# Optimization experiments

Measured on AMD Instinct MI355X. Metric: run time of the kernel, lower is better.

Reference implementation:

```python
import jax, jax.numpy as jnp
import numpy as np

B, N, C, H = 4, 2048, 768, 12
D = C // H  # head_dim = 64


def setup_inputs() -> dict:
    key = jax.random.key(0)
    ks = jax.random.split(key, 16)
    s = 1.0 / np.sqrt(C)
    inp = {
        "x1": jax.random.normal(ks[0], (B, N, C), jnp.float32),
        "x2": jax.random.normal(ks[1], (B, N, C), jnp.float32),
        "mask_1": jax.random.uniform(ks[2], (B, N), jnp.float32),
        "mask_2": jax.random.uniform(ks[3], (B, N), jnp.float32),
        "Wq": jax.random.normal(ks[4], (C, C), jnp.float32) * s,
        "bq": jnp.zeros((C,), jnp.float32),
        "Wk": jax.random.normal(ks[5], (C, C), jnp.float32) * s,
        "bk": jnp.zeros((C,), jnp.float32),
        "Wv": jax.random.normal(ks[6], (C, C), jnp.float32) * s,
        "bv": jnp.zeros((C,), jnp.float32),
        "Wo": jax.random.normal(ks[7], (C, C), jnp.float32) * s,
        "bo": jnp.zeros((C,), jnp.float32),
        "temperature": jnp.asarray(1.0, jnp.float32),
        "ln_gamma": jnp.ones((C,), jnp.float32),
        "ln_beta": jnp.zeros((C,), jnp.float32),
    }
    return inp


def _layernorm(x, gamma, beta, eps=1e-5):
    mu = jnp.mean(x, axis=-1, keepdims=True)
    var = jnp.var(x, axis=-1, keepdims=True)
    return (x - mu) * jax.lax.rsqrt(var + eps) * gamma + beta


def reference(x1, x2, mask_1, mask_2, Wq, bq, Wk, bk, Wv, bv, Wo, bo,
              temperature, ln_gamma, ln_beta):
    # projections (nn.Linear: x @ W^T + b)
    q = (x1 @ Wq.T + bq).reshape(B, N, H, D).transpose(0, 2, 1, 3)  # [B,H,N,D]
    k = (x2 @ Wk.T + bk).reshape(B, N, H, D).transpose(0, 2, 1, 3)
    v = (x2 @ Wv.T + bv).reshape(B, N, H, D).transpose(0, 2, 1, 3)

    scores = jnp.einsum("bhnd,bhmd->bhnm", q, k) / jnp.sqrt(jnp.float32(D))
    # relative confidence bias: (mask_1[b,n] - mask_2[b,m]) / temperature
    rel = (mask_1[:, :, None] - mask_2[:, None, :]) / temperature  # [B,N,N]
    scores = scores + rel[:, None, :, :]

    attn = jax.nn.softmax(scores, axis=-1)  # dropout = identity (eval mode)
    out = jnp.einsum("bhnm,bhmd->bhnd", attn, v)
    out = out.transpose(0, 2, 1, 3).reshape(B, N, C)
    out = out @ Wo.T + bo
    return _layernorm(0.5 * x1 + out, ln_gamma, ln_beta)
```

## Files before the change

kernel.cpp:

```cpp
#include <hip/hip_runtime.h>
#include <stdint.h>

#define B_ 4
#define N_ 2048
#define C_ 768
#define H_ 12
#define D_ 64
#define NTOK 8192

typedef short bf16x8 __attribute__((ext_vector_type(8)));
typedef float f32x4 __attribute__((ext_vector_type(4)));
typedef float f32x16 __attribute__((ext_vector_type(16)));
typedef unsigned short ushort8 __attribute__((ext_vector_type(8)));
typedef unsigned short u16x4 __attribute__((ext_vector_type(4)));

__device__ __forceinline__ unsigned short f2bf(float f) {
  union { float f; unsigned u; } v; v.f = f;
  unsigned r = v.u + 0x7FFFu + ((v.u >> 16) & 1u);
  return (unsigned short)(r >> 16);
}

__device__ __forceinline__ void load_lds16(const void* g, void* lds_base) {
  __builtin_amdgcn_global_load_lds(
      (const __attribute__((address_space(1))) unsigned int*)g,
      (__attribute__((address_space(3))) unsigned int*)(uint32_t)(uintptr_t)lds_base,
      16, 0, 0);
}

__device__ __forceinline__ int key2slot(int key) {
  return ((key >> 5) << 5) | (((key >> 4) & 1) << 4) | (((key >> 2) & 1) << 3)
       | (((key >> 3) & 1) << 2) | (key & 3);
}

__device__ __forceinline__ bf16x8 pack8(const float* p) {
  union { unsigned u[4]; bf16x8 v; } r;
#pragma unroll
  for (int j=0;j<4;j++) {
    union { float f; unsigned u; } a, b;
    a.f = p[2*j]; b.f = p[2*j+1];
    r.u[j] = __builtin_amdgcn_perm(b.u + 0x8000u, a.u + 0x8000u, 0x07060302u);
  }
  return r.v;
}

__global__ __launch_bounds__(256) void cvt6(
    const float* s0, const float* s1, const float* s2, const float* s3,
    const float* s4, const float* s5,
    unsigned short* d0, unsigned short* d1, unsigned short* d2,
    unsigned short* d3, unsigned short* d4, unsigned short* d5,
    int n01, int n25)
{
  int y = blockIdx.y;
  const float* s = (y==0)?s0:(y==1)?s1:(y==2)?s2:(y==3)?s3:(y==4)?s4:s5;
  unsigned short* d = (y==0)?d0:(y==1)?d1:(y==2)?d2:(y==3)?d3:(y==4)?d4:d5;
  int n = (y<2) ? n01 : n25;
  int i = (blockIdx.x*256 + threadIdx.x)*8;
  if (i >= n) return;
  float4 f0 = *(const float4*)(s+i);
  float4 f1 = *(const float4*)(s+i+4);
  ushort8 o;
  o[0]=f2bf(f0.x); o[1]=f2bf(f0.y); o[2]=f2bf(f0.z); o[3]=f2bf(f0.w);
  o[4]=f2bf(f1.x); o[5]=f2bf(f1.y); o[6]=f2bf(f1.z); o[7]=f2bf(f1.w);
  *(ushort8*)(d+i) = o;
}

__device__ __forceinline__ void gemm_core(const unsigned short* A, const unsigned short* W,
                                          int rowBase, int colBase, f32x4 (&acc)[4][4],
                                          unsigned short* As, unsigned short* Bs)
{
  int tid = threadIdx.x, wave = tid>>6, lane = tid&63, quad = lane>>4, l16 = lane&15;
  int wm = wave>>1, wn = wave&1;
  for (int k0 = 0; k0 < 768; k0 += 32) {
    __syncthreads();
#pragma unroll
    for (int p = 0; p < 2; ++p) {
      int c = p*256 + wave*64 + lane;
      load_lds16(A + (size_t)(rowBase + (c>>2))*768 + k0 + (c&3)*8,
                 As + (size_t)(p*256 + wave*64)*8);
      load_lds16(W + (size_t)(colBase + (c>>2))*768 + k0 + (c&3)*8,
                 Bs + (size_t)(p*256 + wave*64)*8);
    }
    __syncthreads();
    bf16x8 af[4], bw[4];
#pragma unroll
    for (int i=0;i<4;i++) af[i] = *(const bf16x8*)(As + (wm*64 + i*16 + l16)*32 + quad*8);
#pragma unroll
    for (int j=0;j<4;j++) bw[j] = *(const bf16x8*)(Bs + (wn*64 + j*16 + l16)*32 + quad*8);
#pragma unroll
    for (int i=0;i<4;i++)
#pragma unroll
      for (int j=0;j<4;j++)
        acc[i][j] = __builtin_amdgcn_mfma_f32_16x16x32_bf16(af[i], bw[j], acc[i][j], 0,0,0);
  }
}

__global__ __launch_bounds__(256) void qkv_gemm(
    const unsigned short* xb1, const unsigned short* xb2,
    const unsigned short* Wq, const unsigned short* Wk, const unsigned short* Wv,
    const float* bq, const float* bk, const float* bv,
    unsigned short* Qb, unsigned short* Kb, unsigned short* Vb)
{
  __shared__ unsigned short SU[64*132];
  unsigned short* As = SU;
  unsigned short* Bs = SU + 4096;
  int z = blockIdx.z;
  const unsigned short* A = (z==0) ? xb1 : xb2;
  const unsigned short* W = (z==0) ? Wq : (z==1) ? Wk : Wv;
  const float* bias       = (z==0) ? bq : (z==1) ? bk : bv;
  unsigned short* out     = (z==0) ? Qb : (z==1) ? Kb : Vb;
  int rowBase = blockIdx.x*128, colBase = blockIdx.y*128;
  int tid = threadIdx.x, wave = tid>>6, lane = tid&63, quad = lane>>4, l16 = lane&15;
  int wm = wave>>1, wn = wave&1;
  f32x4 acc[4][4] = {};
  gemm_core(A, W, rowBase, colBase, acc, As, Bs);
  if (z == 2) {
    unsigned short* T = SU;
    int b = rowBase >> 11, n0 = rowBase & 2047;
#pragma unroll
    for (int phase=0; phase<2; ++phase) {
      __syncthreads();
      if (wn == phase) {
#pragma unroll
        for (int i=0;i<4;i++)
#pragma unroll
          for (int j=0;j<4;j++) {
            int d = j*16 + l16;
            float bv_ = bias[colBase + phase*64 + d];
#pragma unroll
            for (int r=0;r<4;r++) {
              int t = wm*64 + i*16 + quad*4 + r;
              int sl = (t & 64) | key2slot(t & 63);
              T[d*132 + sl] = f2bf(acc[i][j][r] + bv_);
            }
          }
      }
      __syncthreads();
      int h = (colBase >> 6) + phase;
      int row = tid >> 2, seg = tid & 3;
      unsigned short* dst = out + ((size_t)(b*H_ + h)*D_ + row)*N_ + n0 + seg*32;
      const unsigned short* src = T + row*132 + seg*32;
#pragma unroll
      for (int u=0;u<4;u++)
        *(ushort8*)(dst + u*8) = *(const ushort8*)(src + u*8);
    }
  } else {
#pragma unroll
    for (int i=0;i<4;i++)
#pragma unroll
      for (int j=0;j<4;j++) {
        int col = colBase + wn*64 + j*16 + l16;
        float bv_ = bias[col];
        int h = col >> 6, d = col & 63;
#pragma unroll
        for (int r=0;r<4;r++) {
          int m = rowBase + wm*64 + i*16 + quad*4 + r;
          int b = m >> 11, n = m & 2047;
          out[(((size_t)b*H_ + h)*N_ + n)*D_ + d] = f2bf(acc[i][j][r] + bv_);
        }
      }
  }
}

__device__ __forceinline__ void attn_stage(const unsigned short* Kb, const unsigned short* Vtg,
                                           size_t bh, int kt, int tid, int wave,
                                           unsigned short* KsBuf, unsigned short* VsBuf)
{
#pragma unroll
  for (int p=0;p<2;p++) {
    int idx = p*256 + tid;
    int key = idx >> 3, c = idx & 7;
    load_lds16(Kb + (bh*N_ + (size_t)kt*64 + key)*D_ + (c ^ (key & 7))*8,
               KsBuf + (size_t)(p*256 + wave*64)*8);
  }
#pragma unroll
  for (int p=0;p<2;p++) {
    int idx = p*256 + tid;
    int d = idx >> 3, c = idx & 7;
    load_lds16(Vtg + (bh*D_ + d)*(size_t)N_ + kt*64 + (c ^ (d & 7))*8,
               VsBuf + (size_t)(p*256 + wave*64)*8);
  }
}

__global__ __launch_bounds__(256) void attn_kernel(
    const unsigned short* Qb, const unsigned short* Kb, const unsigned short* Vtg,
    const float* mask2, const float* temp,
    unsigned short* Ob)
{
  __shared__ unsigned short Ks[2*64*64];
  __shared__ unsigned short Vs[2*64*64];
  __shared__ float m2x[N_];
  const float LOG2E = 1.4426950408889634f;
  const float SCL = 0.125f * LOG2E;
  int bx = blockIdx.x;
  int xcd = bx & 7, slot = bx >> 3;
  int bh_i = xcd*6 + (slot >> 4);
  int qt = slot & 15;
  int b = bh_i / H_, h = bh_i - b*H_;
  int tid = threadIdx.x, wave = tid>>6, lane = tid&63;
  int l32 = lane & 31, hl = lane >> 5;
  float invT = 1.0f / temp[0];
  size_t bh = (size_t)bh_i;
  int qrow = qt*128 + wave*32 + l32;

#pragma unroll
  for (int r=0;r<8;r++) {
    int i = r*256 + tid;
    m2x[i] = (-mask2[b*N_ + i]*invT - 8.0f) * LOG2E;
  }

  bf16x8 qf[4];
  const unsigned short* Qp = Qb + (bh*N_ + qrow)*D_;
#pragma unroll
  for (int i=0;i<4;i++) qf[i] = *(const bf16x8*)(Qp + i*16 + hl*8);

  int loff[4];
#pragma unroll
  for (int t=0;t<4;t++) loff[t] = l32*64 + (((2*t + hl) ^ (l32 & 7))*8);

  float lrun = 0.f;
  f32x16 oacc0 = {}, oacc1 = {};

  attn_stage(Kb, Vtg, bh, 0, tid, wave, Ks, Vs);
  __syncthreads();

#pragma unroll 2
  for (int kt = 0; kt < N_/64; ++kt) {
    int cur = kt & 1;
    if (kt+1 < N_/64)
      attn_stage(Kb, Vtg, bh, kt+1, tid, wave, Ks + (cur^1)*4096, Vs + (cur^1)*4096);
#pragma unroll
    for (int sub=0; sub<2; ++sub) {
      f32x16 sa = {};
#pragma unroll
      for (int i=0;i<4;i++) {
        bf16x8 kf = *(const bf16x8*)(Ks + cur*4096 + sub*2048 + loff[i]);
        sa = __builtin_amdgcn_mfma_f32_32x32x16_bf16(kf, qf[i], sa, 0,0,0);
      }
      float pv[16];
#pragma unroll
      for (int g=0; g<4; ++g) {
        float4 mv = *(const float4*)(m2x + kt*64 + sub*32 + g*8 + hl*4);
#pragma unroll
        for (int q=0;q<4;q++)
          pv[g*4+q] = __builtin_amdgcn_exp2f(sa[g*4+q]*SCL + ((const float*)&mv)[q]);
      }
      bf16x8 pf0 = pack8(pv);
      bf16x8 pf1 = pack8(pv+8);
#pragma unroll
      for (int kc=0;kc<2;kc++) {
        bf16x8 pf = kc ? pf1 : pf0;
        int m = sub*2 + kc;
        oacc0 = __builtin_amdgcn_mfma_f32_32x32x16_bf16(
                  *(const bf16x8*)(Vs + cur*4096 + loff[m]), pf, oacc0, 0,0,0);
        oacc1 = __builtin_amdgcn_mfma_f32_32x32x16_bf16(
                  *(const bf16x8*)(Vs + cur*4096 + 2048 + loff[m]), pf, oacc1, 0,0,0);
      }
      float rs = 0.f;
#pragma unroll
      for (int r=0;r<16;r++) rs += pv[r];
      lrun += rs;
    }
    __syncthreads();
  }

  lrun += __shfl_xor(lrun, 32);
  float rinv = 1.0f / lrun;
  size_t obase = ((size_t)b*N_ + qrow)*C_ + h*D_;
#pragma unroll
  for (int dh=0; dh<2; ++dh)
#pragma unroll
    for (int g=0; g<4; ++g) {
      int d = dh*32 + g*8 + hl*4;
      u16x4 o;
#pragma unroll
      for (int q=0;q<4;q++) {
        float val = (dh==0 ? oacc0[g*4+q] : oacc1[g*4+q]) * rinv;
        o[q] = f2bf(val);
      }
      *(u16x4*)(Ob + obase + d) = o;
    }
}

__global__ __launch_bounds__(256) void out_gemm(
    const unsigned short* Ob, const unsigned short* Wo, const float* bo,
    const float* x1, float* Z)
{
  __shared__ unsigned short As[128*32];
  __shared__ unsigned short Bs[128*32];
  int rowBase = blockIdx.x*128, colBase = blockIdx.y*128;
  int tid = threadIdx.x, wave = tid>>6, lane = tid&63, quad = lane>>4, l16 = lane&15;
  int wm = wave>>1, wn = wave&1;
  f32x4 acc[4][4] = {};
  gemm_core(Ob, Wo, rowBase, colBase, acc, As, Bs);
#pragma unroll
  for (int i=0;i<4;i++)
#pragma unroll
    for (int j=0;j<4;j++) {
      int col = colBase + wn*64 + j*16 + l16;
      float bv_ = bo[col];
#pragma unroll
      for (int r=0;r<4;r++) {
        size_t m = rowBase + wm*64 + i*16 + quad*4 + r;
        Z[m*768 + col] = acc[i][j][r] + bv_ + 0.5f*x1[m*768 + col];
      }
    }
}

__global__ __launch_bounds__(256) void ln_kernel(const float* Z, const float* gam,
                                                 const float* bet, float* out)
{
  size_t row = blockIdx.x;
  int t = threadIdx.x;
  const float* z = Z + row*768;
  float v0 = z[t], v1 = z[t+256], v2 = z[t+512];
  float s = v0+v1+v2;
  float ss = v0*v0 + v1*v1 + v2*v2;
#pragma unroll
  for (int off=1; off<64; off<<=1) { s += __shfl_xor(s, off); ss += __shfl_xor(ss, off); }
  __shared__ float red[8];
  int wave = t>>6, lane = t&63;
  if (lane==0) { red[wave] = s; red[4+wave] = ss; }
  __syncthreads();
  float S = red[0]+red[1]+red[2]+red[3];
  float SS = red[4]+red[5]+red[6]+red[7];
  float mean = S * (1.0f/768.0f);
  float var = SS * (1.0f/768.0f) - mean*mean;
  float rstd = rsqrtf(var + 1e-5f);
  float* o = out + row*768;
  o[t]     = (v0-mean)*rstd*gam[t]     + bet[t];
  o[t+256] = (v1-mean)*rstd*gam[t+256] + bet[t+256];
  o[t+512] = (v2-mean)*rstd*gam[t+512] + bet[t+512];
}

extern "C" void kernel_launch(void* const* d_in, const int* in_sizes, int n_in,
                              void* d_out, int out_size, void* d_ws, size_t ws_size,
                              hipStream_t stream)
{
  const float* x1    = (const float*)d_in[0];
  const float* x2    = (const float*)d_in[1];
  const float* mask2 = (const float*)d_in[3];
  const float* Wq    = (const float*)d_in[4];
  const float* bq    = (const float*)d_in[5];
  const float* Wk    = (const float*)d_in[6];
  const float* bk    = (const float*)d_in[7];
  const float* Wv    = (const float*)d_in[8];
  const float* bv    = (const float*)d_in[9];
  const float* Wo    = (const float*)d_in[10];
  const float* bo    = (const float*)d_in[11];
  const float* temp  = (const float*)d_in[12];
  const float* gam   = (const float*)d_in[13];
  const float* bet   = (const float*)d_in[14];

  char* ws = (char*)d_ws;
  size_t off = 0;
  auto alloc = [&](size_t bytes) { void* p = ws + off; off += (bytes + 255) & ~255ull; return p; };
  const size_t XB = (size_t)NTOK * C_ * 2;
  const size_t WB = (size_t)C_ * C_ * 2;
  unsigned short* xb1 = (unsigned short*)alloc(XB);
  unsigned short* xb2 = (unsigned short*)alloc(XB);
  unsigned short* Wqb = (unsigned short*)alloc(WB);
  unsigned short* Wkb = (unsigned short*)alloc(WB);
  unsigned short* Wvb = (unsigned short*)alloc(WB);
  unsigned short* Wob = (unsigned short*)alloc(WB);
  unsigned short* Qb  = (unsigned short*)alloc(XB);
  unsigned short* Kb  = (unsigned short*)alloc(XB);
  unsigned short* Vb  = (unsigned short*)alloc(XB);
  unsigned short* Ob  = (unsigned short*)alloc(XB);
  float* Z = (float*)xb1;

  cvt6<<<dim3(3072, 6), 256, 0, stream>>>(x1, x2, Wq, Wk, Wv, Wo,
                                          xb1, xb2, Wqb, Wkb, Wvb, Wob,
                                          NTOK*C_, C_*C_);
  qkv_gemm<<<dim3(64, 6, 3), 256, 0, stream>>>(xb1, xb2, Wqb, Wkb, Wvb,
                                               bq, bk, bv, Qb, Kb, Vb);
  attn_kernel<<<dim3(768), 256, 0, stream>>>(Qb, Kb, Vb, mask2, temp, Ob);
  out_gemm<<<dim3(64, 6), 256, 0, stream>>>(Ob, Wob, bo, x1, Z);
  ln_kernel<<<dim3(8192), 256, 0, stream>>>(Z, gam, bet, (float*)d_out);
}
```

Before: 294.0 us.

## Widen GEMM K-tile to 64 with XOR-swizzled LDS and trim attention packing

The shared GEMM core now stages 64-wide K slices with an XOR swizzle on 16-byte chunks. This halves the barrier and loop count and is meant to avoid LDS bank conflicts on the fragment reads, at the cost of doubled LDS per block. In attention, bf16 packing now truncates instead of rounding, swizzled offsets are computed inline rather than precomputed, and the row-sum uses paired float2 adds. The truncation slightly lowers precision of the probability weights.

After: 316.0 us. 1.07x slower.

```diff
diff --git a/kernel.cpp b/kernel.cpp
--- a/kernel.cpp
+++ b/kernel.cpp
@@ -11,6 +11,7 @@
 typedef short bf16x8 __attribute__((ext_vector_type(8)));
 typedef float f32x4 __attribute__((ext_vector_type(4)));
 typedef float f32x16 __attribute__((ext_vector_type(16)));
+typedef float f32x2v __attribute__((ext_vector_type(2)));
 typedef unsigned short ushort8 __attribute__((ext_vector_type(8)));
 typedef unsigned short u16x4 __attribute__((ext_vector_type(4)));
 
@@ -32,13 +33,13 @@
        | (((key >> 3) & 1) << 2) | (key & 3);
 }
 
-__device__ __forceinline__ bf16x8 pack8(const float* p) {
+__device__ __forceinline__ bf16x8 pack8t(const float* p) {
   union { unsigned u[4]; bf16x8 v; } r;
 #pragma unroll
   for (int j=0;j<4;j++) {
     union { float f; unsigned u; } a, b;
     a.f = p[2*j]; b.f = p[2*j+1];
-    r.u[j] = __builtin_amdgcn_perm(b.u + 0x8000u, a.u + 0x8000u, 0x07060302u);
+    r.u[j] = __builtin_amdgcn_perm(b.u, a.u, 0x07060302u);
   }
   return r.v;
 }
@@ -70,27 +71,39 @@
 {
   int tid = threadIdx.x, wave = tid>>6, lane = tid&63, quad = lane>>4, l16 = lane&15;
   int wm = wave>>1, wn = wave&1;
-  for (int k0 = 0; k0 < 768; k0 += 32) {
+  for (int k0 = 0; k0 < 768; k0 += 64) {
     __syncthreads();
 #pragma unroll
-    for (int p = 0; p < 2; ++p) {
-      int c = p*256 + wave*64 + lane;
-      load_lds16(A + (size_t)(rowBase + (c>>2))*768 + k0 + (c&3)*8,
+    for (int p = 0; p < 4; ++p) {
+      int idx = p*256 + tid;
+      int row = idx >> 3, c = idx & 7;
+      load_lds16(A + (size_t)(rowBase + row)*768 + k0 + ((c ^ (row & 7))*8),
                  As + (size_t)(p*256 + wave*64)*8);
-      load_lds16(W + (size_t)(colBase + (c>>2))*768 + k0 + (c&3)*8,
+      load_lds16(W + (size_t)(colBase + row)*768 + k0 + ((c ^ (row & 7))*8),
                  Bs + (size_t)(p*256 + wave*64)*8);
     }
     __syncthreads();
-    bf16x8 af[4], bw[4];
-#pragma unroll
-    for (int i=0;i<4;i++) af[i] = *(const bf16x8*)(As + (wm*64 + i*16 + l16)*32 + quad*8);
-#pragma unroll
-    for (int j=0;j<4;j++) bw[j] = *(const bf16x8*)(Bs + (wn*64 + j*16 + l16)*32 + quad*8);
-#pragma unroll
-    for (int i=0;i<4;i++)
-#pragma unroll
-      for (int j=0;j<4;j++)
-        acc[i][j] = __builtin_amdgcn_mfma_f32_16x16x32_bf16(af[i], bw[j], acc[i][j], 0,0,0);
+#pragma unroll
+    for (int h=0; h<2; ++h) {
+      bf16x8 af[4], bw[4];
+#pragma unroll
+      for (int i=0;i<4;i++) {
+        int row = wm*64 + i*16 + l16;
+        int ch = (h*4 + quad) ^ (row & 7);
+        af[i] = *(const bf16x8*)(As + row*64 + ch*8);
+      }
+#pragma unroll
+      for (int j=0;j<4;j++) {
+        int row = wn*64 + j*16 + l16;
+        int ch = (h*4 + quad) ^ (row & 7);
+        bw[j] = *(const bf16x8*)(Bs + row*64 + ch*8);
+      }
+#pragma unroll
+      for (int i=0;i<4;i++)
+#pragma unroll
+        for (int j=0;j<4;j++)
+          acc[i][j] = __builtin_amdgcn_mfma_f32_16x16x32_bf16(af[i], bw[j], acc[i][j], 0,0,0);
+    }
   }
 }
 
@@ -100,9 +113,9 @@
     const float* bq, const float* bk, const float* bv,
     unsigned short* Qb, unsigned short* Kb, unsigned short* Vb)
 {
-  __shared__ unsigned short SU[64*132];
+  __shared__ unsigned short SU[2*128*64];
   unsigned short* As = SU;
-  unsigned short* Bs = SU + 4096;
+  unsigned short* Bs = SU + 128*64;
   int z = blockIdx.z;
   const unsigned short* A = (z==0) ? xb1 : xb2;
   const unsigned short* W = (z==0) ? Wq : (z==1) ? Wk : Wv;
@@ -186,8 +199,8 @@
     const float* mask2, const float* temp,
     unsigned short* Ob)
 {
-  __shared__ unsigned short Ks[2*64*64];
-  __shared__ unsigned short Vs[2*64*64];
+  __shared__ unsigned short Ks[2][64*64];
+  __shared__ unsigned short Vs[2][64*64];
   __shared__ float m2x[N_];
   const float LOG2E = 1.4426950408889634f;
   const float SCL = 0.125f * LOG2E;
@@ -213,27 +226,25 @@
 #pragma unroll
   for (int i=0;i<4;i++) qf[i] = *(const bf16x8*)(Qp + i*16 + hl*8);
 
-  int loff[4];
-#pragma unroll
-  for (int t=0;t<4;t++) loff[t] = l32*64 + (((2*t + hl) ^ (l32 & 7))*8);
-
   float lrun = 0.f;
   f32x16 oacc0 = {}, oacc1 = {};
 
-  attn_stage(Kb, Vtg, bh, 0, tid, wave, Ks, Vs);
+  attn_stage(Kb, Vtg, bh, 0, tid, wave, Ks[0], Vs[0]);
   __syncthreads();
 
-#pragma unroll 2
   for (int kt = 0; kt < N_/64; ++kt) {
     int cur = kt & 1;
     if (kt+1 < N_/64)
-      attn_stage(Kb, Vtg, bh, kt+1, tid, wave, Ks + (cur^1)*4096, Vs + (cur^1)*4096);
+      attn_stage(Kb, Vtg, bh, kt+1, tid, wave, Ks[cur^1], Vs[cur^1]);
+    const unsigned short* Kc = Ks[cur];
+    const unsigned short* Vc = Vs[cur];
 #pragma unroll
     for (int sub=0; sub<2; ++sub) {
       f32x16 sa = {};
 #pragma unroll
       for (int i=0;i<4;i++) {
-        bf16x8 kf = *(const bf16x8*)(Ks + cur*4096 + sub*2048 + loff[i]);
+        int ch = (2*i + hl) ^ (l32 & 7);
+        bf16x8 kf = *(const bf16x8*)(Kc + (sub*32 + l32)*64 + ch*8);
         sa = __builtin_amdgcn_mfma_f32_32x32x16_bf16(kf, qf[i], sa, 0,0,0);
       }
       float pv[16];
@@ -244,21 +255,23 @@
         for (int q=0;q<4;q++)
           pv[g*4+q] = __builtin_amdgcn_exp2f(sa[g*4+q]*SCL + ((const float*)&mv)[q]);
       }
-      bf16x8 pf0 = pack8(pv);
-      bf16x8 pf1 = pack8(pv+8);
+      bf16x8 pf0 = pack8t(pv);
+      bf16x8 pf1 = pack8t(pv+8);
 #pragma unroll
       for (int kc=0;kc<2;kc++) {
         bf16x8 pf = kc ? pf1 : pf0;
         int m = sub*2 + kc;
+        int chv = (2*m + hl) ^ (l32 & 7);
         oacc0 = __builtin_amdgcn_mfma_f32_32x32x16_bf16(
-                  *(const bf16x8*)(Vs + cur*4096 + loff[m]), pf, oacc0, 0,0,0);
+                  *(const bf16x8*)(Vc + l32*64 + chv*8), pf, oacc0, 0,0,0);
+        int chv1 = (2*m + hl) ^ ((32+l32) & 7);
         oacc1 = __builtin_amdgcn_mfma_f32_32x32x16_bf16(
-                  *(const bf16x8*)(Vs + cur*4096 + 2048 + loff[m]), pf, oacc1, 0,0,0);
-      }
-      float rs = 0.f;
-#pragma unroll
-      for (int r=0;r<16;r++) rs += pv[r];
-      lrun += rs;
+                  *(const bf16x8*)(Vc + (32+l32)*64 + chv1*8), pf, oacc1, 0,0,0);
+      }
+      f32x2v rs2 = {0.f, 0.f};
+#pragma unroll
+      for (int r=0;r<8;r++) rs2 += *(const f32x2v*)(pv + 2*r);
+      lrun += rs2[0] + rs2[1];
     }
     __syncthreads();
   }
@@ -285,8 +298,8 @@
     const unsigned short* Ob, const unsigned short* Wo, const float* bo,
     const float* x1, float* Z)
 {
-  __shared__ unsigned short As[128*32];
-  __shared__ unsigned short Bs[128*32];
+  __shared__ unsigned short As[128*64];
+  __shared__ unsigned short Bs[128*64];
   int rowBase = blockIdx.x*128, colBase = blockIdx.y*128;
   int tid = threadIdx.x, wave = tid>>6, lane = tid&63, quad = lane>>4, l16 = lane&15;
   int wm = wave>>1, wn = wave&1;
```
